# Performance work log

Hardware: AMD Instinct MI355X
Metric: run time of the kernel (lower is better)

## Reference

```python
import jax, jax.numpy as jnp
import numpy as np

EPS = 1e-05


def setup_inputs() -> dict:
    key = jax.random.key(0)
    ks = jax.random.split(key, 7)
    N, C_in, H, W = 32, 64, 128, 128
    C_out, K = 128, 3
    x = jax.random.normal(ks[0], (N, C_in, H, W), dtype=jnp.float32)
    weight = jax.random.normal(ks[1], (C_out, C_in, K, K), dtype=jnp.float32) * 0.05
    bias = jax.random.normal(ks[2], (C_out,), dtype=jnp.float32) * 0.1
    gamma = jax.random.uniform(ks[3], (C_out,), dtype=jnp.float32, minval=0.5, maxval=1.5)
    beta = jax.random.normal(ks[4], (C_out,), dtype=jnp.float32) * 0.1
    running_mean = jax.random.normal(ks[5], (C_out,), dtype=jnp.float32) * 0.1
    running_var = jax.random.uniform(ks[6], (C_out,), dtype=jnp.float32, minval=0.5, maxval=1.5)
    return {"x": x, "weight": weight, "bias": bias, "gamma": gamma,
            "beta": beta, "running_mean": running_mean, "running_var": running_var}


def reference(x, weight, bias, gamma, beta, running_mean, running_var):
    # conv2d, stride=1, VALID padding, NCHW / OIHW
    z = jax.lax.conv_general_dilated(
        x, weight, window_strides=(1, 1), padding='VALID',
        dimension_numbers=('NCHW', 'OIHW', 'NCHW'))
    z = z + bias[None, :, None, None]
    # mish-like: z * tanh(softplus(z))
    z = z * jnp.tanh(jax.nn.softplus(z))
    # BatchNorm inference folded to per-channel affine
    scale = gamma / jnp.sqrt(running_var + EPS)
    shift = beta - running_mean * scale
    return z * scale[None, :, None, None] + shift[None, :, None, None]
```

## Files before the change

kernel.cpp:

```cpp
#include <hip/hip_runtime.h>

typedef unsigned int  u32;
typedef unsigned short u16;
typedef __attribute__((ext_vector_type(8))) short short8;
typedef __attribute__((ext_vector_type(4))) float f32x4;

#define CI 64
#define CO 128
#define HH 128
#define WW 128
#define HO 126
#define WO 126

__device__ __forceinline__ u16 f2bf(float f) {
    u32 u = __builtin_bit_cast(u32, f);
    u = (u + 0x7FFFu + ((u >> 16) & 1u)) >> 16;
    return (u16)u;
}

__global__ void reorder_w(const float* __restrict__ w, u16* __restrict__ wq) {
    int i = blockIdx.x * 256 + threadIdx.x;
    if (i < 9 * CO * CI) {
        int ci  = i & 63;
        int co  = (i >> 6) & 127;
        int tap = i >> 13;
        wq[i] = f2bf(w[(co * CI + ci) * 9 + tap]);
    }
}

__global__ __launch_bounds__(256)
void prep_x(const float* __restrict__ x, u16* __restrict__ xq) {
    __shared__ float lf[64 * 128];
    const int row = blockIdx.x;
    const int n = row >> 7, h = row & 127;
    const float* xb = x + (size_t)n * CI * HH * WW + (size_t)h * WW;

    const int w4  = threadIdx.x & 31;
    const int ci0 = threadIdx.x >> 5;
#pragma unroll
    for (int it = 0; it < 8; ++it) {
        int ci = it * 8 + ci0;
        f32x4 v = *(const f32x4*)(xb + (size_t)ci * (HH * WW) + w4 * 4);
        int s = (ci >> 3) ^ (ci & 7);
        *(f32x4*)&lf[ci * 128 + ((w4 ^ s) * 4)] = v;
    }
    __syncthreads();

    u16* dst = xq + (size_t)row * 8192;
#pragma unroll
    for (int it = 0; it < 4; ++it) {
        int idx  = it * 256 + threadIdx.x;
        int slot = idx & 7;
        int w    = idx >> 3;
        int g    = slot ^ (w & 7);
        int wq4  = w >> 2, wr = w & 3;
        u32 parts[4];
#pragma unroll
        for (int jj = 0; jj < 4; ++jj) {
            int ca = g * 8 + 2 * jj;
            int cb = ca + 1;
            float va = lf[ca * 128 + ((wq4 ^ ((ca >> 3) ^ (ca & 7))) * 4) + wr];
            float vb = lf[cb * 128 + ((wq4 ^ ((cb >> 3) ^ (cb & 7))) * 4) + wr];
            parts[jj] = (u32)f2bf(va) | ((u32)f2bf(vb) << 16);
        }
        uint4 q;
        q.x = parts[0]; q.y = parts[1]; q.z = parts[2]; q.w = parts[3];
        *(uint4*)(dst + (size_t)w * 64 + slot * 8) = q;
    }
}

__global__ __launch_bounds__(256, 2)
void conv_mfma_v4(const u16* __restrict__ xq, const u16* __restrict__ wq,
                  const float* __restrict__ bias, const float* __restrict__ gamma,
                  const float* __restrict__ beta, const float* __restrict__ rmean,
                  const float* __restrict__ rvar, float* __restrict__ out) {
    __shared__ u16 in_lds[3 * 128 * 64];
    __shared__ float s_scale[CO], s_shift[CO], s_bias[CO];

    const int tid = threadIdx.x;
    const int D = blockIdx.y * 126 + blockIdx.x;
    const int L = (D & 7) * 504 + (D >> 3);
    const int n  = L / 126;
    const int h0 = L - n * 126;

    const int wv   = tid >> 6;
    const int lane = tid & 63;
    const u16* src = xq + (size_t)(n * 128 + h0) * 8192;
#pragma unroll
    for (int s = 0; s < 12; ++s) {
        int chunk = s * 4 + wv;
        const u16* gp = src + chunk * 512 + lane * 8;
        u16*       lp = in_lds + chunk * 512 + lane * 8;
        __builtin_amdgcn_global_load_lds(
            (const __attribute__((address_space(1))) u32*)gp,
            (__attribute__((address_space(3))) u32*)lp, 16, 0, 0);
    }

    if (tid < CO) {
        float sc = gamma[tid] * rsqrtf(rvar[tid] + 1e-5f);
        s_scale[tid] = sc;
        s_shift[tid] = beta[tid] - rmean[tid] * sc;
        s_bias[tid]  = bias[tid];
    }
    __syncthreads();

    const int li = tid & 15;
    const int qd = (tid & 63) >> 4;
    const int wm = wv & 1;
    const int wn = wv >> 1;

    f32x4 zero4 = {0.f, 0.f, 0.f, 0.f};
    f32x4 acc[4][4];
#pragma unroll
    for (int i = 0; i < 4; ++i)
#pragma unroll
        for (int j = 0; j < 4; ++j) acc[i][j] = zero4;

    const uint4* wg = (const uint4*)wq;

#pragma unroll 1
    for (int kh = 0; kh < 3; ++kh) {
#pragma unroll
        for (int kw = 0; kw < 3; ++kw) {
            const int tap = kh * 3 + kw;
#pragma unroll
            for (int ks = 0; ks < 2; ++ks) {
                short8 a[4], b[4];
#pragma unroll
                for (int i = 0; i < 4; ++i) {
                    int co = wm * 64 + i * 16 + li;
                    a[i] = __builtin_bit_cast(short8,
                        wg[tap * 1024 + co * 8 + ks * 4 + qd]);
                }
#pragma unroll
                for (int j = 0; j < 4; ++j) {
                    int w = wn * 64 + j * 16 + li + kw;
                    int g = ks * 4 + qd;
                    b[j] = *(const short8*)&in_lds[(size_t)(kh * 128 + w) * 64 +
                                                   ((g ^ (w & 7)) * 8)];
                }
#pragma unroll
                for (int i = 0; i < 4; ++i)
#pragma unroll
                    for (int j = 0; j < 4; ++j)
                        acc[i][j] = __builtin_amdgcn_mfma_f32_16x16x32_bf16(
                            b[j], a[i], acc[i][j], 0, 0, 0);
            }
        }
    }

    const bool al16 = ((h0 & 1) == 0);
    float* ob = out + (size_t)n * CO * (HO * WO) + (size_t)h0 * WO;
#pragma unroll
    for (int i = 0; i < 4; ++i) {
        int co = wm * 64 + i * 16 + li;
        float sc = s_scale[co], sh = s_shift[co], bs = s_bias[co];
        float* op = ob + (size_t)co * (HO * WO);
#pragma unroll
        for (int j = 0; j < 4; ++j) {
            int wo0 = wn * 64 + j * 16 + qd * 4;
            f32x4 v;
#pragma unroll
            for (int r = 0; r < 4; ++r) {
                float z  = acc[i][j][r] + bs;
                float u  = 1.0f + __expf(fminf(z, 20.0f));
                float u2 = u * u;
                float t  = __fdividef(u2 - 1.0f, u2 + 1.0f);
                v[r] = z * t * sc + sh;
            }
            if (wo0 + 3 < WO) {
                if (al16) {
                    *(f32x4*)(op + wo0) = v;
                } else {
                    float2 t0; t0.x = v[0]; t0.y = v[1];
                    float2 t1; t1.x = v[2]; t1.y = v[3];
                    *(float2*)(op + wo0)     = t0;
                    *(float2*)(op + wo0 + 2) = t1;
                }
            } else {
#pragma unroll
                for (int r = 0; r < 4; ++r)
                    if (wo0 + r < WO) op[wo0 + r] = v[r];
            }
        }
    }
}

__global__ __launch_bounds__(256, 2)
void conv_mfma(const float* __restrict__ x, const u16* __restrict__ wq,
               const float* __restrict__ bias, const float* __restrict__ gamma,
               const float* __restrict__ beta, const float* __restrict__ rmean,
               const float* __restrict__ rvar, float* __restrict__ out) {
    __shared__ u32 in_lds[3 * 130 * 32];
    __shared__ float s_scale[CO], s_shift[CO], s_bias[CO];

    const int tid = threadIdx.x;
    const int h0  = blockIdx.x;
    const int n   = blockIdx.y;

    if (tid < CO) {
        float sc = gamma[tid] * rsqrtf(rvar[tid] + 1e-5f);
        s_scale[tid] = sc;
        s_shift[tid] = beta[tid] - rmean[tid] * sc;
        s_bias[tid]  = bias[tid];
    }
    if (tid < 48) {
        int kh  = tid >> 4;
        int rem = tid & 15;
        int w   = 128 + (rem & 1);
        int g   = rem >> 1;
        uint4 z = {0u, 0u, 0u, 0u};
        *(uint4*)&in_lds[(kh * 130 + w) * 32 + ((g ^ (w & 7)) * 4)] = z;
    }
    const float* xb = x + (size_t)n * CI * HH * WW;
    for (int it = 0; it < 12; ++it) {
        int idx = it * 256 + tid;
        int w   = idx & 127;
        int g   = (idx >> 7) & 7;
        int kh  = idx >> 10;
        const float* p = xb + (g * 8) * (HH * WW) + (h0 + kh) * WW + w;
        float v[8];
#pragma unroll
        for (int j = 0; j < 8; ++j) v[j] = p[j * (HH * WW)];
        uint4 q;
        q.x = (u32)f2bf(v[0]) | ((u32)f2bf(v[1]) << 16);
        q.y = (u32)f2bf(v[2]) | ((u32)f2bf(v[3]) << 16);
        q.z = (u32)f2bf(v[4]) | ((u32)f2bf(v[5]) << 16);
        q.w = (u32)f2bf(v[6]) | ((u32)f2bf(v[7]) << 16);
        *(uint4*)&in_lds[(kh * 130 + w) * 32 + ((g ^ (w & 7)) * 4)] = q;
    }
    __syncthreads();

    const int wv = tid >> 6;
    const int li = tid & 15;
    const int qd = (tid & 63) >> 4;
    const int wm = wv & 1;
    const int wn = wv >> 1;

    f32x4 zero4 = {0.f, 0.f, 0.f, 0.f};
    f32x4 acc[4][4];
#pragma unroll
    for (int i = 0; i < 4; ++i)
#pragma unroll
        for (int j = 0; j < 4; ++j) acc[i][j] = zero4;

    const uint4* wg = (const uint4*)wq;

#pragma unroll 1
    for (int kh = 0; kh < 3; ++kh) {
#pragma unroll
        for (int kw = 0; kw < 3; ++kw) {
            const int tap = kh * 3 + kw;
#pragma unroll
            for (int ks = 0; ks < 2; ++ks) {
                short8 a[4], b[4];
#pragma unroll
                for (int i = 0; i < 4; ++i) {
                    int co = wm * 64 + i * 16 + li;
                    a[i] = __builtin_bit_cast(short8,
                        wg[tap * 1024 + co * 8 + ks * 4 + qd]);
                }
#pragma unroll
                for (int j = 0; j < 4; ++j) {
                    int w = wn * 64 + j * 16 + li + kw;
                    int g = ks * 4 + qd;
                    b[j] = *(const short8*)&in_lds[(kh * 130 + w) * 32 +
                                                   ((g ^ (w & 7)) * 4)];
                }
#pragma unroll
                for (int i = 0; i < 4; ++i)
#pragma unroll
                    for (int j = 0; j < 4; ++j)
                        acc[i][j] = __builtin_amdgcn_mfma_f32_16x16x32_bf16(
                            a[i], b[j], acc[i][j], 0, 0, 0);
            }
        }
    }

    float* ob = out + (size_t)n * CO * (HO * WO) + (size_t)h0 * WO;
#pragma unroll
    for (int j = 0; j < 4; ++j) {
        int wo = wn * 64 + j * 16 + li;
        if (wo < WO) {
#pragma unroll
            for (int i = 0; i < 4; ++i) {
#pragma unroll
                for (int r = 0; r < 4; ++r) {
                    int co  = wm * 64 + i * 16 + qd * 4 + r;
                    float z  = acc[i][j][r] + s_bias[co];
                    float u  = 1.0f + __expf(fminf(z, 20.0f));
                    float u2 = u * u;
                    float t  = __fdividef(u2 - 1.0f, u2 + 1.0f);
                    ob[(size_t)co * (HO * WO) + wo] = z * t * s_scale[co] + s_shift[co];
                }
            }
        }
    }
}

extern "C" void kernel_launch(void* const* d_in, const int* in_sizes, int n_in,
                              void* d_out, int out_size, void* d_ws, size_t ws_size,
                              hipStream_t stream) {
    const float* x     = (const float*)d_in[0];
    const float* wt    = (const float*)d_in[1];
    const float* bias  = (const float*)d_in[2];
    const float* gamma = (const float*)d_in[3];
    const float* beta  = (const float*)d_in[4];
    const float* rmean = (const float*)d_in[5];
    const float* rvar  = (const float*)d_in[6];

    const size_t XQ_BYTES = (size_t)64 * 1024 * 1024;
    const size_t WQ_BYTES = (size_t)9 * CO * CI * 2;

    if (ws_size >= XQ_BYTES + WQ_BYTES) {
        u16* xq = (u16*)d_ws;
        u16* wq = (u16*)((char*)d_ws + XQ_BYTES);
        hipLaunchKernelGGL(reorder_w, dim3(288), dim3(256), 0, stream, wt, wq);
        hipLaunchKernelGGL(prep_x, dim3(4096), dim3(256), 0, stream, x, xq);
        hipLaunchKernelGGL(conv_mfma_v4, dim3(HO, 32), dim3(256), 0, stream,
                           xq, wq, bias, gamma, beta, rmean, rvar, (float*)d_out);
    } else {
        u16* wq = (u16*)d_ws;
        hipLaunchKernelGGL(reorder_w, dim3(288), dim3(256), 0, stream, wt, wq);
        hipLaunchKernelGGL(conv_mfma, dim3(HO, 32), dim3(256), 0, stream,
                           x, wq, bias, gamma, beta, rmean, rvar, (float*)d_out);
    }
}
```

Measured before the change: 526.6 us.

## Precompute swizzled LDS addresses, batch weight loads per kh, raise occupancy

Precomputes the XOR-swizzled LDS byte addresses for the B fragments once, before the barrier, and reorders the main loop so each ks step loads the weight fragments for all three kw taps at once. The kh loop is now fully unrolled and launch bounds go up to three blocks per SM. The aim is to cut address arithmetic in the inner loop, expose more memory-level parallelism for the global weight loads, and hide latency with more resident waves. The cost is extra register pressure from the aw[3][4] buffer and the address table, which under the tighter occupancy bound could cause spills.

```diff
diff --git a/kernel.cpp b/kernel.cpp
--- a/kernel.cpp
+++ b/kernel.cpp
@@ -69,8 +69,8 @@
     }
 }
 
-__global__ __launch_bounds__(256, 2)
-void conv_mfma_v4(const u16* __restrict__ xq, const u16* __restrict__ wq,
+__global__ __launch_bounds__(256, 3)
+void conv_mfma_v5(const u16* __restrict__ xq, const u16* __restrict__ wq,
                   const float* __restrict__ bias, const float* __restrict__ gamma,
                   const float* __restrict__ beta, const float* __restrict__ rmean,
                   const float* __restrict__ rvar, float* __restrict__ out) {
@@ -102,13 +102,25 @@
         s_shift[tid] = beta[tid] - rmean[tid] * sc;
         s_bias[tid]  = bias[tid];
     }
-    __syncthreads();
 
     const int li = tid & 15;
     const int qd = (tid & 63) >> 4;
     const int wm = wv & 1;
     const int wn = wv >> 1;
 
+    u32 baddr[4][3];
+#pragma unroll
+    for (int j = 0; j < 4; ++j)
+#pragma unroll
+        for (int kw = 0; kw < 3; ++kw) {
+            int w  = wn * 64 + j * 16 + li + kw;
+            int s  = w & 7;
+            int g0 = (qd ^ (s & 3)) + 4 * (s >> 2);
+            baddr[j][kw] = (u32)(w * 128 + g0 * 16);
+        }
+
+    __syncthreads();
+
     f32x4 zero4 = {0.f, 0.f, 0.f, 0.f};
     f32x4 acc[4][4];
 #pragma unroll
@@ -116,35 +128,33 @@
 #pragma unroll
         for (int j = 0; j < 4; ++j) acc[i][j] = zero4;
 
-    const uint4* wg = (const uint4*)wq;
-
-#pragma unroll 1
+    const uint4* wp = (const uint4*)wq + (wm * 512 + li * 8 + qd);
+    const char*  lb = (const char*)in_lds;
+
+#pragma unroll
     for (int kh = 0; kh < 3; ++kh) {
 #pragma unroll
-        for (int kw = 0; kw < 3; ++kw) {
-            const int tap = kh * 3 + kw;
-#pragma unroll
-            for (int ks = 0; ks < 2; ++ks) {
-                short8 a[4], b[4];
-#pragma unroll
-                for (int i = 0; i < 4; ++i) {
-                    int co = wm * 64 + i * 16 + li;
-                    a[i] = __builtin_bit_cast(short8,
-                        wg[tap * 1024 + co * 8 + ks * 4 + qd]);
-                }
-#pragma unroll
-                for (int j = 0; j < 4; ++j) {
-                    int w = wn * 64 + j * 16 + li + kw;
-                    int g = ks * 4 + qd;
-                    b[j] = *(const short8*)&in_lds[(size_t)(kh * 128 + w) * 64 +
-                                                   ((g ^ (w & 7)) * 8)];
-                }
+        for (int ks = 0; ks < 2; ++ks) {
+            const u32 ksx = (u32)(ks << 6);
+            short8 aw[3][4];
+#pragma unroll
+            for (int kw = 0; kw < 3; ++kw)
+#pragma unroll
+                for (int i = 0; i < 4; ++i)
+                    aw[kw][i] = __builtin_bit_cast(short8,
+                        wp[(kh * 3 + kw) * 1024 + i * 128 + ks * 4]);
+#pragma unroll
+            for (int kw = 0; kw < 3; ++kw) {
+                short8 b[4];
+#pragma unroll
+                for (int j = 0; j < 4; ++j)
+                    b[j] = *(const short8*)(lb + ((baddr[j][kw] ^ ksx) + kh * 16384));
 #pragma unroll
                 for (int i = 0; i < 4; ++i)
 #pragma unroll
                     for (int j = 0; j < 4; ++j)
                         acc[i][j] = __builtin_amdgcn_mfma_f32_16x16x32_bf16(
-                            b[j], a[i], acc[i][j], 0, 0, 0);
+                            b[j], aw[kw][i], acc[i][j], 0, 0, 0);
             }
         }
     }
@@ -317,7 +327,7 @@
         u16* wq = (u16*)((char*)d_ws + XQ_BYTES);
         hipLaunchKernelGGL(reorder_w, dim3(288), dim3(256), 0, stream, wt, wq);
         hipLaunchKernelGGL(prep_x, dim3(4096), dim3(256), 0, stream, x, xq);
-        hipLaunchKernelGGL(conv_mfma_v4, dim3(HO, 32), dim3(256), 0, stream,
+        hipLaunchKernelGGL(conv_mfma_v5, dim3(HO, 32), dim3(256), 0, stream,
                            xq, wq, bias, gamma, beta, rmean, rvar, (float*)d_out);
     } else {
         u16* wq = (u16*)d_ws;
```

After: 521.5 us. No clear change (-1.0%).

## Make conv kernel persistent with DMA prefetch of next row overlapping epilogue

Applied to the files above, without the earlier changes.

The conv kernel now launches 768 persistent blocks, each processing 5-6 consecutive output rows. After the MMA loop it issues the async global-to-LDS load for the next row, so that load overlaps the mish/BN epilogue and output stores. prep_x and reorder_w are also coarsened to handle 8 rows or 4 elements per block, cutting block launch overhead. The trade-off is fewer resident blocks, less latency hiding across blocks, and possible tail imbalance from the uneven 5 or 6 row counts.

```diff
diff --git a/kernel.cpp b/kernel.cpp
--- a/kernel.cpp
+++ b/kernel.cpp
@@ -19,8 +19,10 @@
 }
 
 __global__ void reorder_w(const float* __restrict__ w, u16* __restrict__ wq) {
-    int i = blockIdx.x * 256 + threadIdx.x;
-    if (i < 9 * CO * CI) {
+    int base = blockIdx.x * 1024 + threadIdx.x;
+#pragma unroll
+    for (int t = 0; t < 4; ++t) {
+        int i   = base + t * 256;
         int ci  = i & 63;
         int co  = (i >> 6) & 127;
         int tap = i >> 13;
@@ -31,46 +33,50 @@
 __global__ __launch_bounds__(256)
 void prep_x(const float* __restrict__ x, u16* __restrict__ xq) {
     __shared__ float lf[64 * 128];
-    const int row = blockIdx.x;
-    const int n = row >> 7, h = row & 127;
-    const float* xb = x + (size_t)n * CI * HH * WW + (size_t)h * WW;
-
     const int w4  = threadIdx.x & 31;
     const int ci0 = threadIdx.x >> 5;
-#pragma unroll
-    for (int it = 0; it < 8; ++it) {
-        int ci = it * 8 + ci0;
-        f32x4 v = *(const f32x4*)(xb + (size_t)ci * (HH * WW) + w4 * 4);
-        int s = (ci >> 3) ^ (ci & 7);
-        *(f32x4*)&lf[ci * 128 + ((w4 ^ s) * 4)] = v;
-    }
-    __syncthreads();
-
-    u16* dst = xq + (size_t)row * 8192;
-#pragma unroll
-    for (int it = 0; it < 4; ++it) {
-        int idx  = it * 256 + threadIdx.x;
-        int slot = idx & 7;
-        int w    = idx >> 3;
-        int g    = slot ^ (w & 7);
-        int wq4  = w >> 2, wr = w & 3;
-        u32 parts[4];
-#pragma unroll
-        for (int jj = 0; jj < 4; ++jj) {
-            int ca = g * 8 + 2 * jj;
-            int cb = ca + 1;
-            float va = lf[ca * 128 + ((wq4 ^ ((ca >> 3) ^ (ca & 7))) * 4) + wr];
-            float vb = lf[cb * 128 + ((wq4 ^ ((cb >> 3) ^ (cb & 7))) * 4) + wr];
-            parts[jj] = (u32)f2bf(va) | ((u32)f2bf(vb) << 16);
-        }
-        uint4 q;
-        q.x = parts[0]; q.y = parts[1]; q.z = parts[2]; q.w = parts[3];
-        *(uint4*)(dst + (size_t)w * 64 + slot * 8) = q;
+
+    for (int t = 0; t < 8; ++t) {
+        const int row = blockIdx.x * 8 + t;
+        const int n = row >> 7, h = row & 127;
+        const float* xb = x + (size_t)n * CI * HH * WW + (size_t)h * WW;
+
+#pragma unroll
+        for (int it = 0; it < 8; ++it) {
+            int ci = it * 8 + ci0;
+            f32x4 v = *(const f32x4*)(xb + (size_t)ci * (HH * WW) + w4 * 4);
+            int s = (ci >> 3) ^ (ci & 7);
+            *(f32x4*)&lf[ci * 128 + ((w4 ^ s) * 4)] = v;
+        }
+        __syncthreads();
+
+        u16* dst = xq + (size_t)row * 8192;
+#pragma unroll
+        for (int it = 0; it < 4; ++it) {
+            int idx  = it * 256 + threadIdx.x;
+            int slot = idx & 7;
+            int w    = idx >> 3;
+            int g    = slot ^ (w & 7);
+            int wq4  = w >> 2, wr = w & 3;
+            u32 parts[4];
+#pragma unroll
+            for (int jj = 0; jj < 4; ++jj) {
+                int ca = g * 8 + 2 * jj;
+                int cb = ca + 1;
+                float va = lf[ca * 128 + ((wq4 ^ ((ca >> 3) ^ (ca & 7))) * 4) + wr];
+                float vb = lf[cb * 128 + ((wq4 ^ ((cb >> 3) ^ (cb & 7))) * 4) + wr];
+                parts[jj] = (u32)f2bf(va) | ((u32)f2bf(vb) << 16);
+            }
+            uint4 q;
+            q.x = parts[0]; q.y = parts[1]; q.z = parts[2]; q.w = parts[3];
+            *(uint4*)(dst + (size_t)w * 64 + slot * 8) = q;
+        }
+        __syncthreads();
     }
 }
 
 __global__ __launch_bounds__(256, 2)
-void conv_mfma_v4(const u16* __restrict__ xq, const u16* __restrict__ wq,
+void conv_mfma_v6(const u16* __restrict__ xq, const u16* __restrict__ wq,
                   const float* __restrict__ bias, const float* __restrict__ gamma,
                   const float* __restrict__ beta, const float* __restrict__ rmean,
                   const float* __restrict__ rvar, float* __restrict__ out) {
@@ -78,23 +84,14 @@
     __shared__ float s_scale[CO], s_shift[CO], s_bias[CO];
 
     const int tid = threadIdx.x;
-    const int D = blockIdx.y * 126 + blockIdx.x;
-    const int L = (D & 7) * 504 + (D >> 3);
-    const int n  = L / 126;
-    const int h0 = L - n * 126;
+    const int k = blockIdx.x & 7;
+    const int l = blockIdx.x >> 3;
+    const int lmin = (l < 24) ? l : 24;
+    const int start = k * 504 + l * 5 + lmin;
+    const int cnt   = 5 + (l < 24 ? 1 : 0);
 
     const int wv   = tid >> 6;
     const int lane = tid & 63;
-    const u16* src = xq + (size_t)(n * 128 + h0) * 8192;
-#pragma unroll
-    for (int s = 0; s < 12; ++s) {
-        int chunk = s * 4 + wv;
-        const u16* gp = src + chunk * 512 + lane * 8;
-        u16*       lp = in_lds + chunk * 512 + lane * 8;
-        __builtin_amdgcn_global_load_lds(
-            (const __attribute__((address_space(1))) u32*)gp,
-            (__attribute__((address_space(3))) u32*)lp, 16, 0, 0);
-    }
 
     if (tid < CO) {
         float sc = gamma[tid] * rsqrtf(rvar[tid] + 1e-5f);
@@ -102,85 +99,112 @@
         s_shift[tid] = beta[tid] - rmean[tid] * sc;
         s_bias[tid]  = bias[tid];
     }
-    __syncthreads();
+
+    auto issue_dma = [&](int u) {
+        int n  = u / 126;
+        int h0 = u - n * 126;
+        const u16* src = xq + (size_t)(n * 128 + h0) * 8192;
+#pragma unroll
+        for (int s = 0; s < 12; ++s) {
+            int chunk = s * 4 + wv;
+            const u16* gp = src + chunk * 512 + lane * 8;
+            u16*       lp = in_lds + chunk * 512 + lane * 8;
+            __builtin_amdgcn_global_load_lds(
+                (const __attribute__((address_space(1))) u32*)gp,
+                (__attribute__((address_space(3))) u32*)lp, 16, 0, 0);
+        }
+    };
 
     const int li = tid & 15;
     const int qd = (tid & 63) >> 4;
     const int wm = wv & 1;
     const int wn = wv >> 1;
 
-    f32x4 zero4 = {0.f, 0.f, 0.f, 0.f};
-    f32x4 acc[4][4];
-#pragma unroll
-    for (int i = 0; i < 4; ++i)
-#pragma unroll
-        for (int j = 0; j < 4; ++j) acc[i][j] = zero4;
-
     const uint4* wg = (const uint4*)wq;
+    const f32x4 zero4 = {0.f, 0.f, 0.f, 0.f};
+
+    issue_dma(start);
+
+    for (int t = 0; t < cnt; ++t) {
+        const int u  = start + t;
+        const int n  = u / 126;
+        const int h0 = u - n * 126;
+
+        __syncthreads();
+
+        f32x4 acc[4][4];
+#pragma unroll
+        for (int i = 0; i < 4; ++i)
+#pragma unroll
+            for (int j = 0; j < 4; ++j) acc[i][j] = zero4;
 
 #pragma unroll 1
-    for (int kh = 0; kh < 3; ++kh) {
-#pragma unroll
-        for (int kw = 0; kw < 3; ++kw) {
-            const int tap = kh * 3 + kw;
-#pragma unroll
-            for (int ks = 0; ks < 2; ++ks) {
-                short8 a[4], b[4];
-#pragma unroll
-                for (int i = 0; i < 4; ++i) {
-                    int co = wm * 64 + i * 16 + li;
-                    a[i] = __builtin_bit_cast(short8,
-                        wg[tap * 1024 + co * 8 + ks * 4 + qd]);
-                }
-#pragma unroll
-                for (int j = 0; j < 4; ++j) {
-                    int w = wn * 64 + j * 16 + li + kw;
-                    int g = ks * 4 + qd;
-                    b[j] = *(const short8*)&in_lds[(size_t)(kh * 128 + w) * 64 +
-                                                   ((g ^ (w & 7)) * 8)];
-                }
-#pragma unroll
-                for (int i = 0; i < 4; ++i)
-#pragma unroll
-                    for (int j = 0; j < 4; ++j)
-                        acc[i][j] = __builtin_amdgcn_mfma_f32_16x16x32_bf16(
-                            b[j], a[i], acc[i][j], 0, 0, 0);
-            }
-        }
-    }
-
-    const bool al16 = ((h0 & 1) == 0);
-    float* ob = out + (size_t)n * CO * (HO * WO) + (size_t)h0 * WO;
-#pragma unroll
-    for (int i = 0; i < 4; ++i) {
-        int co = wm * 64 + i * 16 + li;
-        float sc = s_scale[co], sh = s_shift[co], bs = s_bias[co];
-        float* op = ob + (size_t)co * (HO * WO);
-#pragma unroll
-        for (int j = 0; j < 4; ++j) {
-            int wo0 = wn * 64 + j * 16 + qd * 4;
-            f32x4 v;
-#pragma unroll
-            for (int r = 0; r < 4; ++r) {
-                float z  = acc[i][j][r] + bs;
-                float u  = 1.0f + __expf(fminf(z, 20.0f));
-                float u2 = u * u;
-                float t  = __fdividef(u2 - 1.0f, u2 + 1.0f);
-                v[r] = z * t * sc + sh;
-            }
-            if (wo0 + 3 < WO) {
-                if (al16) {
-                    *(f32x4*)(op + wo0) = v;
+        for (int kh = 0; kh < 3; ++kh) {
+#pragma unroll
+            for (int kw = 0; kw < 3; ++kw) {
+                const int tap = kh * 3 + kw;
+#pragma unroll
+                for (int ks = 0; ks < 2; ++ks) {
+                    short8 a[4], b[4];
+#pragma unroll
+                    for (int i = 0; i < 4; ++i) {
+                        int co = wm * 64 + i * 16 + li;
+                        a[i] = __builtin_bit_cast(short8,
+                            wg[tap * 1024 + co * 8 + ks * 4 + qd]);
+                    }
+#pragma unroll
+                    for (int j = 0; j < 4; ++j) {
+                        int w = wn * 64 + j * 16 + li + kw;
+                        int g = ks * 4 + qd;
+                        b[j] = *(const short8*)&in_lds[(size_t)(kh * 128 + w) * 64 +
+                                                       ((g ^ (w & 7)) * 8)];
+                    }
+#pragma unroll
+                    for (int i = 0; i < 4; ++i)
+#pragma unroll
+                        for (int j = 0; j < 4; ++j)
+                            acc[i][j] = __builtin_amdgcn_mfma_f32_16x16x32_bf16(
+                                b[j], a[i], acc[i][j], 0, 0, 0);
+                }
+            }
+        }
+
+        __syncthreads();
+        if (t + 1 < cnt) issue_dma(u + 1);
+
+        const bool al16 = ((h0 & 1) == 0);
+        float* ob = out + (size_t)n * CO * (HO * WO) + (size_t)h0 * WO;
+#pragma unroll
+        for (int i = 0; i < 4; ++i) {
+            int co = wm * 64 + i * 16 + li;
+            float sc = s_scale[co], sh = s_shift[co], bs = s_bias[co];
+            float* op = ob + (size_t)co * (HO * WO);
+#pragma unroll
+            for (int j = 0; j < 4; ++j) {
+                int wo0 = wn * 64 + j * 16 + qd * 4;
+                f32x4 v;
+#pragma unroll
+                for (int r = 0; r < 4; ++r) {
+                    float z  = acc[i][j][r] + bs;
+                    float u1 = 1.0f + __expf(fminf(z, 20.0f));
+                    float u2 = u1 * u1;
+                    float tt = __fdividef(u2 - 1.0f, u2 + 1.0f);
+                    v[r] = z * tt * sc + sh;
+                }
+                if (wo0 + 3 < WO) {
+                    if (al16) {
+                        *(f32x4*)(op + wo0) = v;
+                    } else {
+                        float2 t0; t0.x = v[0]; t0.y = v[1];
+                        float2 t1; t1.x = v[2]; t1.y = v[3];
+                        *(float2*)(op + wo0)     = t0;
+                        *(float2*)(op + wo0 + 2) = t1;
+                    }
                 } else {
-                    float2 t0; t0.x = v[0]; t0.y = v[1];
-                    float2 t1; t1.x = v[2]; t1.y = v[3];
-                    *(float2*)(op + wo0)     = t0;
-                    *(float2*)(op + wo0 + 2) = t1;
-                }
-            } else {
-#pragma unroll
-                for (int r = 0; r < 4; ++r)
-                    if (wo0 + r < WO) op[wo0 + r] = v[r];
+#pragma unroll
+                    for (int r = 0; r < 4; ++r)
+                        if (wo0 + r < WO) op[wo0 + r] = v[r];
+                }
             }
         }
     }
@@ -315,9 +339,9 @@
     if (ws_size >= XQ_BYTES + WQ_BYTES) {
         u16* xq = (u16*)d_ws;
         u16* wq = (u16*)((char*)d_ws + XQ_BYTES);
-        hipLaunchKernelGGL(reorder_w, dim3(288), dim3(256), 0, stream, wt, wq);
-        hipLaunchKernelGGL(prep_x, dim3(4096), dim3(256), 0, stream, x, xq);
-        hipLaunchKernelGGL(conv_mfma_v4, dim3(HO, 32), dim3(256), 0, stream,
+        hipLaunchKernelGGL(reorder_w, dim3(72), dim3(256), 0, stream, wt, wq);
+        hipLaunchKernelGGL(prep_x, dim3(512), dim3(256), 0, stream, x, xq);
+        hipLaunchKernelGGL(conv_mfma_v6, dim3(768), dim3(256), 0, stream,
                            xq, wq, bias, gamma, beta, rmean, rvar, (float*)d_out);
     } else {
         u16* wq = (u16*)d_ws;
```

Result: slower. 585.3 us (+11.1%).

## Split conv tiles into half-width blocks with smaller LDS and higher occupancy

Applied to the files above, without the earlier changes.

Each workgroup now computes half an output row (64 columns) for all 128 output channels, with each wave owning 32 channels instead of a 64x64 quadrant. The LDS input tile shrinks to 3x72 columns, the grid doubles to 8064 one-dimensional blocks with a remapped swizzle, and launch bounds go up to 5 blocks per CU. The aim is more occupancy and better latency hiding. In exchange, input rows are loaded with a small overlap between halves, weight reuse per block is lower, and each wave issues fewer MFMAs per B-fragment load.

```diff
diff --git a/kernel.cpp b/kernel.cpp
--- a/kernel.cpp
+++ b/kernel.cpp
@@ -69,31 +69,41 @@
     }
 }
 
-__global__ __launch_bounds__(256, 2)
-void conv_mfma_v4(const u16* __restrict__ xq, const u16* __restrict__ wq,
+__global__ __launch_bounds__(256, 5)
+void conv_mfma_v7(const u16* __restrict__ xq, const u16* __restrict__ wq,
                   const float* __restrict__ bias, const float* __restrict__ gamma,
                   const float* __restrict__ beta, const float* __restrict__ rmean,
                   const float* __restrict__ rvar, float* __restrict__ out) {
-    __shared__ u16 in_lds[3 * 128 * 64];
+    __shared__ u16 in_lds[3 * 72 * 64];
     __shared__ float s_scale[CO], s_shift[CO], s_bias[CO];
 
     const int tid = threadIdx.x;
-    const int D = blockIdx.y * 126 + blockIdx.x;
-    const int L = (D & 7) * 504 + (D >> 3);
-    const int n  = L / 126;
-    const int h0 = L - n * 126;
+    const int D = blockIdx.x;
+    const int L = (D & 7) * 1008 + (D >> 3);
+    const int g  = L / 126;
+    const int h0 = L - g * 126;
+    const int n    = g >> 1;
+    const int half = g & 1;
+    const int W0   = half * 64;
+    const int ws0  = half * 56;
+    const int woff = half * 8;
 
     const int wv   = tid >> 6;
     const int lane = tid & 63;
-    const u16* src = xq + (size_t)(n * 128 + h0) * 8192;
-#pragma unroll
-    for (int s = 0; s < 12; ++s) {
-        int chunk = s * 4 + wv;
-        const u16* gp = src + chunk * 512 + lane * 8;
-        u16*       lp = in_lds + chunk * 512 + lane * 8;
-        __builtin_amdgcn_global_load_lds(
-            (const __attribute__((address_space(1))) u32*)gp,
-            (__attribute__((address_space(3))) u32*)lp, 16, 0, 0);
+
+    const u16* src = xq + (size_t)(n * 128 + h0) * 8192 + ws0 * 64;
+#pragma unroll
+    for (int s = 0; s < 7; ++s) {
+        int c = s * 4 + wv;
+        if (c < 27) {
+            int r  = (c >= 18) ? 2 : ((c >= 9) ? 1 : 0);
+            int cr = c - r * 9;
+            const u16* gp = src + (size_t)r * 8192 + cr * 512 + lane * 8;
+            u16*       lp = in_lds + r * 4608 + cr * 512 + lane * 8;
+            __builtin_amdgcn_global_load_lds(
+                (const __attribute__((address_space(1))) u32*)gp,
+                (__attribute__((address_space(3))) u32*)lp, 16, 0, 0);
+        }
     }
 
     if (tid < CO) {
@@ -106,17 +116,15 @@
 
     const int li = tid & 15;
     const int qd = (tid & 63) >> 4;
-    const int wm = wv & 1;
-    const int wn = wv >> 1;
 
     f32x4 zero4 = {0.f, 0.f, 0.f, 0.f};
-    f32x4 acc[4][4];
-#pragma unroll
-    for (int i = 0; i < 4; ++i)
+    f32x4 acc[2][4];
+#pragma unroll
+    for (int i = 0; i < 2; ++i)
 #pragma unroll
         for (int j = 0; j < 4; ++j) acc[i][j] = zero4;
 
-    const uint4* wg = (const uint4*)wq;
+    const uint4* wp = (const uint4*)wq + ((wv * 32 + li) * 8 + qd);
 
 #pragma unroll 1
     for (int kh = 0; kh < 3; ++kh) {
@@ -125,22 +133,20 @@
             const int tap = kh * 3 + kw;
 #pragma unroll
             for (int ks = 0; ks < 2; ++ks) {
-                short8 a[4], b[4];
-#pragma unroll
-                for (int i = 0; i < 4; ++i) {
-                    int co = wm * 64 + i * 16 + li;
+                short8 a[2], b[4];
+#pragma unroll
+                for (int i = 0; i < 2; ++i)
                     a[i] = __builtin_bit_cast(short8,
-                        wg[tap * 1024 + co * 8 + ks * 4 + qd]);
-                }
+                        wp[tap * 1024 + i * 128 + ks * 4]);
 #pragma unroll
                 for (int j = 0; j < 4; ++j) {
-                    int w = wn * 64 + j * 16 + li + kw;
-                    int g = ks * 4 + qd;
-                    b[j] = *(const short8*)&in_lds[(size_t)(kh * 128 + w) * 64 +
-                                                   ((g ^ (w & 7)) * 8)];
-                }
-#pragma unroll
-                for (int i = 0; i < 4; ++i)
+                    int wl = woff + j * 16 + li + kw;
+                    int gg = ks * 4 + qd;
+                    b[j] = *(const short8*)&in_lds[(kh * 72 + wl) * 64 +
+                                                   ((gg ^ (wl & 7)) * 8)];
+                }
+#pragma unroll
+                for (int i = 0; i < 2; ++i)
 #pragma unroll
                     for (int j = 0; j < 4; ++j)
                         acc[i][j] = __builtin_amdgcn_mfma_f32_16x16x32_bf16(
@@ -150,15 +156,16 @@
     }
 
     const bool al16 = ((h0 & 1) == 0);
-    float* ob = out + (size_t)n * CO * (HO * WO) + (size_t)h0 * WO;
-#pragma unroll
-    for (int i = 0; i < 4; ++i) {
-        int co = wm * 64 + i * 16 + li;
+    float* ob = out + (size_t)n * CO * (HO * WO) + (size_t)h0 * WO + W0;
+#pragma unroll
+    for (int i = 0; i < 2; ++i) {
+        int co = wv * 32 + i * 16 + li;
         float sc = s_scale[co], sh = s_shift[co], bs = s_bias[co];
         float* op = ob + (size_t)co * (HO * WO);
 #pragma unroll
         for (int j = 0; j < 4; ++j) {
-            int wo0 = wn * 64 + j * 16 + qd * 4;
+            int lo  = j * 16 + qd * 4;
+            int wo0 = W0 + lo;
             f32x4 v;
 #pragma unroll
             for (int r = 0; r < 4; ++r) {
@@ -170,17 +177,17 @@
             }
             if (wo0 + 3 < WO) {
                 if (al16) {
-                    *(f32x4*)(op + wo0) = v;
+                    *(f32x4*)(op + lo) = v;
                 } else {
                     float2 t0; t0.x = v[0]; t0.y = v[1];
                     float2 t1; t1.x = v[2]; t1.y = v[3];
-                    *(float2*)(op + wo0)     = t0;
-                    *(float2*)(op + wo0 + 2) = t1;
+                    *(float2*)(op + lo)     = t0;
+                    *(float2*)(op + lo + 2) = t1;
                 }
             } else {
 #pragma unroll
                 for (int r = 0; r < 4; ++r)
-                    if (wo0 + r < WO) op[wo0 + r] = v[r];
+                    if (wo0 + r < WO) op[lo + r] = v[r];
             }
         }
     }
@@ -317,7 +324,7 @@
         u16* wq = (u16*)((char*)d_ws + XQ_BYTES);
         hipLaunchKernelGGL(reorder_w, dim3(288), dim3(256), 0, stream, wt, wq);
         hipLaunchKernelGGL(prep_x, dim3(4096), dim3(256), 0, stream, x, xq);
-        hipLaunchKernelGGL(conv_mfma_v4, dim3(HO, 32), dim3(256), 0, stream,
+        hipLaunchKernelGGL(conv_mfma_v7, dim3(8064), dim3(256), 0, stream,
                            xq, wq, bias, gamma, beta, rmean, rvar, (float*)d_out);
     } else {
         u16* wq = (u16*)d_ws;
```

Result: slower. 560.2 us (+6.4%).
